# Kernel tuning notes

Hardware: AMD Instinct MI355X
Metric: run time of the kernel (lower is better)

The kernel has to match this reference:

```python
import jax, jax.numpy as jnp
import numpy as np

C = 512
NUM_HEADS = 8
NUM_GROUPS = 32
EPS = 1e-6


def group_norm(x, gamma, beta):
    # x: [B, C, N]
    b, c, n = x.shape
    xg = x.reshape(b, NUM_GROUPS, (c // NUM_GROUPS) * n)
    mean = xg.mean(axis=-1, keepdims=True)
    var = xg.var(axis=-1, keepdims=True)
    xg = (xg - mean) * jax.lax.rsqrt(var + EPS)
    x = xg.reshape(b, c, n)
    return x * gamma[None, :, None] + beta[None, :, None]


def conv1x1(x, w, bias):
    # pointwise conv: w [out_c, in_c], x [B, C, N]
    return jnp.einsum('oc,bcn->bon', w, x) + bias[None, :, None]


def setup_inputs() -> dict:
    key = jax.random.key(0)
    ks = jax.random.split(key, 11)
    s = 1.0 / np.sqrt(C)
    inp = {
        'x': jax.random.normal(ks[0], (4, C, 2048), dtype=jnp.float32),
        'gn_gamma': jnp.ones((C,), jnp.float32),
        'gn_beta': jnp.zeros((C,), jnp.float32),
        'q_w': jax.random.uniform(ks[1], (C, C), jnp.float32, -s, s),
        'q_b': jax.random.uniform(ks[2], (C,), jnp.float32, -s, s),
        'k_w': jax.random.uniform(ks[3], (C, C), jnp.float32, -s, s),
        'k_b': jax.random.uniform(ks[4], (C,), jnp.float32, -s, s),
        'v_w': jax.random.uniform(ks[5], (C, C), jnp.float32, -s, s),
        'v_b': jax.random.uniform(ks[6], (C,), jnp.float32, -s, s),
        'proj_w': jax.random.uniform(ks[7], (C, C), jnp.float32, -s, s),
        'proj_b': jax.random.uniform(ks[8], (C,), jnp.float32, -s, s),
    }
    return inp


def reference(x, gn_gamma, gn_beta, q_w, q_b, k_w, k_b, v_w, v_b, proj_w, proj_b):
    b, c, n = x.shape
    hc = c // NUM_HEADS
    h_ = group_norm(x, gn_gamma, gn_beta)
    q = conv1x1(h_, q_w, q_b)
    k = conv1x1(h_, k_w, k_b)
    v = conv1x1(h_, v_w, v_b)
    # split heads: [B, H, hc, N]
    q = q.reshape(b, NUM_HEADS, hc, n)
    k = k.reshape(b, NUM_HEADS, hc, n)
    v = v.reshape(b, NUM_HEADS, hc, n)
    # NOTE: scale uses full channel count c, matching the original code
    scale = jnp.asarray(c, x.dtype) ** -0.5
    # scores: [B, H, Nq, Nk]
    w = jnp.einsum('bhcn,bhcm->bhnm', q, k) * scale
    w = jax.nn.softmax(w, axis=-1)
    # out[b,h,c,q] = sum_m v[b,h,c,m] * w[b,h,q,m]
    out = jnp.einsum('bhcm,bhqm->bhcq', v, w)
    out = out.reshape(b, c, n)
    out = conv1x1(out, proj_w, proj_b)
    return x + out
```

## Files before the change

### kernel.cpp

```cpp
#include <hip/hip_runtime.h>
#include <hip/hip_bf16.h>
#include <math.h>

#define C_DIM 512
#define N_DIM 2048
#define B_DIM 4
#define NGRP 32
#define GCH 16
#define NHEAD 8
#define HDIM 64
#define EPSV 1e-6f

using f32x4  = __attribute__((ext_vector_type(4))) float;
using bf16x8 = __attribute__((ext_vector_type(8))) short;

#define GLL16(gp, lp) __builtin_amdgcn_global_load_lds( \
    (const __attribute__((address_space(1))) unsigned int*)(gp), \
    (__attribute__((address_space(3))) unsigned int*)(lp), 16, 0, 0)

#define BFPACK(a, b) __builtin_amdgcn_perm(__float_as_uint(b), __float_as_uint(a), 0x07060302u)

static __device__ __forceinline__ unsigned short f2bf(float f) {
    union { __hip_bfloat16 h; unsigned short u; } cv;
    cv.h = __float2bfloat16(f);
    return cv.u;
}

__global__ __launch_bounds__(256) void gn_stats(const float* __restrict__ x,
                                                float* __restrict__ partial) {
    const int HSZ = GCH * N_DIM / 2;
    int blk = blockIdx.x;
    const float4* x4 = (const float4*)(x + (size_t)blk * HSZ);
    int tid = threadIdx.x;

    float s = 0.f, ss = 0.f;
    #pragma unroll
    for (int it = 0; it < HSZ / 4 / 256; ++it) {
        float4 v = x4[tid + it * 256];
        s  += v.x + v.y + v.z + v.w;
        ss += v.x * v.x + v.y * v.y + v.z * v.z + v.w * v.w;
    }
    __shared__ float rs[256], rss[256];
    rs[tid] = s; rss[tid] = ss;
    __syncthreads();
    for (int off = 128; off > 0; off >>= 1) {
        if (tid < off) { rs[tid] += rs[tid + off]; rss[tid] += rss[tid + off]; }
        __syncthreads();
    }
    if (tid == 0) {
        partial[blk * 2]     = rs[0];
        partial[blk * 2 + 1] = rss[0];
    }
}

__global__ __launch_bounds__(256) void gn_apply_t(const float* __restrict__ x,
                                                  const float* __restrict__ partial,
                                                  const float* __restrict__ gamma,
                                                  const float* __restrict__ beta,
                                                  unsigned short* __restrict__ ht) {
    __shared__ char smem[8192];
    const float GSZI = 1.f / (GCH * N_DIM);
    int n0 = blockIdx.x * 64, c0 = blockIdx.y * 64, b = blockIdx.z;
    int tid = threadIdx.x;
    #pragma unroll
    for (int it = 0; it < 4; ++it) {
        int idx = tid + it * 256;
        int ci = idx >> 4, n4 = (idx & 15) << 2;
        int cg = c0 + ci, grp = cg >> 4;
        int bg = b * NGRP + grp;
        float s  = partial[bg * 4]     + partial[bg * 4 + 2];
        float ss = partial[bg * 4 + 1] + partial[bg * 4 + 3];
        float mean = s * GSZI;
        float var  = ss * GSZI - mean * mean;
        float rstd = rsqrtf(var + EPSV);
        float ga = gamma[cg] * rstd, be = beta[cg] - mean * ga;
        float4 v = *(const float4*)&x[((size_t)b * C_DIM + cg) * N_DIM + n0 + n4];
        float vals[4] = {v.x, v.y, v.z, v.w};
        #pragma unroll
        for (int j = 0; j < 4; ++j) {
            int nl = n4 + j;
            *(unsigned short*)(smem + nl * 128 + ((ci * 2) ^ ((nl & 7) << 4))) =
                f2bf(vals[j] * ga + be);
        }
    }
    __syncthreads();
    #pragma unroll
    for (int i = 0; i < 2; ++i) {
        int idx = tid + i * 256;
        int row = idx >> 3, ch = idx & 7;
        bf16x8 v = *(const bf16x8*)(smem + row * 128 + ((ch * 16) ^ ((row & 7) << 4)));
        *(bf16x8*)&ht[((size_t)(b * N_DIM + n0 + row)) * C_DIM + c0 + ch * 8] = v;
    }
}

__global__ __launch_bounds__(256) void cast4_bf16(const float* __restrict__ s0,
                                                  const float* __restrict__ s1,
                                                  const float* __restrict__ s2,
                                                  const float* __restrict__ s3,
                                                  unsigned short* __restrict__ dst) {
    int which = blockIdx.y;
    const float* src = (which == 0) ? s0 : (which == 1) ? s1 : (which == 2) ? s2 : s3;
    size_t idx = (size_t)blockIdx.x * 256 + threadIdx.x;
    const float4* s4 = (const float4*)src;
    float4 a = s4[idx * 2], b = s4[idx * 2 + 1];
    bf16x8 o;
    o[0] = (short)f2bf(a.x); o[1] = (short)f2bf(a.y);
    o[2] = (short)f2bf(a.z); o[3] = (short)f2bf(a.w);
    o[4] = (short)f2bf(b.x); o[5] = (short)f2bf(b.y);
    o[6] = (short)f2bf(b.z); o[7] = (short)f2bf(b.w);
    *(bf16x8*)&dst[(size_t)which * 262144 + idx * 8] = o;
}

__global__ __launch_bounds__(512) void conv_qkv(const unsigned short* __restrict__ Wall,
                                                const float* __restrict__ q_b,
                                                const float* __restrict__ k_b,
                                                const float* __restrict__ v_b,
                                                const unsigned short* __restrict__ ht,
                                                unsigned short* __restrict__ qt,
                                                unsigned short* __restrict__ kt,
                                                unsigned short* __restrict__ vt,
                                                float escale) {
    __shared__ char smem[40960];

    int bn0 = blockIdx.x * 128;
    int bo  = blockIdx.y * 64;
    int tid = threadIdx.x;
    int L = tid & 63, w = tid >> 6;
    int g = L >> 4, c = L & 15;
    int wr = w >> 2, wc = w & 3;

    f32x4 acc[3][2][2];
    #pragma unroll
    for (int w3 = 0; w3 < 3; ++w3)
        #pragma unroll
        for (int t = 0; t < 2; ++t)
            #pragma unroll
            for (int u = 0; u < 2; ++u) acc[w3][t][u] = f32x4{0.f, 0.f, 0.f, 0.f};

    for (int k0 = 0; k0 < C_DIM; k0 += 64) {
        if (w < 4) {
            #pragma unroll
            for (int i = 0; i < 4; ++i) {
                int j = w * 4 + i;
                int row = j * 8 + (L >> 3);
                int sl = (L & 7) ^ (row & 7);
                GLL16(ht + (size_t)(bn0 + row) * C_DIM + k0 + sl * 8, smem + j * 1024);
            }
        } else {
            #pragma unroll
            for (int i = 0; i < 6; ++i) {
                int j = (w - 4) * 6 + i;
                int w3 = j >> 3, jj = j & 7;
                int row = jj * 8 + (L >> 3);
                int sl = (L & 7) ^ (row & 7);
                GLL16(Wall + (size_t)w3 * 262144 + (size_t)(bo + row) * C_DIM + k0 + sl * 8,
                      smem + 16384 + j * 1024);
            }
        }
        __syncthreads();

        bf16x8 bfr[2][2];
        #pragma unroll
        for (int u = 0; u < 2; ++u) {
            int row = wc * 32 + u * 16 + c;
            #pragma unroll
            for (int ks = 0; ks < 2; ++ks)
                bfr[u][ks] = *(const bf16x8*)(smem + row * 128 +
                                              ((g * 16 + ks * 64) ^ ((row & 7) << 4)));
        }
        #pragma unroll
        for (int w3 = 0; w3 < 3; ++w3) {
            char* As = smem + 16384 + w3 * 8192;
            bf16x8 af[2][2];
            #pragma unroll
            for (int t = 0; t < 2; ++t) {
                int row = wr * 32 + t * 16 + c;
                #pragma unroll
                for (int ks = 0; ks < 2; ++ks)
                    af[t][ks] = *(const bf16x8*)(As + row * 128 +
                                                 ((g * 16 + ks * 64) ^ ((row & 7) << 4)));
            }
            #pragma unroll
            for (int ks = 0; ks < 2; ++ks)
                #pragma unroll
                for (int t = 0; t < 2; ++t)
                    #pragma unroll
                    for (int u = 0; u < 2; ++u)
                        acc[w3][t][u] = __builtin_amdgcn_mfma_f32_16x16x32_bf16(
                            af[t][ks], bfr[u][ks], acc[w3][t][u], 0, 0, 0);
        }
        __syncthreads();
    }

    int b  = bn0 >> 11;
    int nb = bn0 & (N_DIM - 1);
    int hh = bo >> 6;
    int bh = b * NHEAD + hh;

    #pragma unroll
    for (int t = 0; t < 2; ++t)
        #pragma unroll
        for (int r = 0; r < 4; ++r) {
            int m = bo + wr * 32 + t * 16 + g * 4 + r;
            float bi = v_b[m];
            #pragma unroll
            for (int u = 0; u < 2; ++u) {
                int n = nb + wc * 32 + u * 16 + c;
                vt[((size_t)b * C_DIM + m) * N_DIM + n] = f2bf(acc[2][t][u][r] + bi);
            }
        }

    char* Ts = smem;
    #pragma unroll
    for (int pass = 0; pass < 2; ++pass) {
        const float* bias = pass ? k_b : q_b;
        float esc = pass ? 1.0f : escale;
        unsigned short* dst = pass ? kt : qt;
        __syncthreads();
        #pragma unroll
        for (int t = 0; t < 2; ++t)
            #pragma unroll
            for (int r = 0; r < 4; ++r) {
                int ml = wr * 32 + t * 16 + g * 4 + r;
                float bi = bias[bo + ml];
                #pragma unroll
                for (int u = 0; u < 2; ++u) {
                    int nl = wc * 32 + u * 16 + c;
                    *(unsigned short*)(Ts + nl * 128 + ((ml * 2) ^ ((nl & 7) << 4))) =
                        f2bf((acc[pass][t][u][r] + bi) * esc);
                }
            }
        __syncthreads();
        #pragma unroll
        for (int i = 0; i < 2; ++i) {
            int idx = tid + i * 512;
            int row = idx >> 3, ch = idx & 7;
            bf16x8 v = *(const bf16x8*)(Ts + row * 128 + ((ch * 16) ^ ((row & 7) << 4)));
            *(bf16x8*)&dst[((size_t)bh * N_DIM + nb + row) * HDIM + ch * 8] = v;
        }
    }
}

__global__ __launch_bounds__(256) void conv_proj(const unsigned short* __restrict__ Wb,
                                                 const float* __restrict__ bias,
                                                 const unsigned short* __restrict__ Bsrc,
                                                 const float* __restrict__ res,
                                                 float* __restrict__ outf) {
    __shared__ char smem[24576];
    int bn0 = blockIdx.x * 128;
    int bo  = blockIdx.y * 64;
    int tid = threadIdx.x;
    int L = tid & 63, w = tid >> 6;
    int g = L >> 4, c = L & 15;
    int wr = w >> 1, wc = w & 1;

    f32x4 acc[2][4];
    #pragma unroll
    for (int t = 0; t < 2; ++t)
        #pragma unroll
        for (int u = 0; u < 4; ++u) acc[t][u] = f32x4{0.f, 0.f, 0.f, 0.f};

    for (int k0 = 0; k0 < C_DIM; k0 += 64) {
        #pragma unroll
        for (int i = 0; i < 2; ++i) {
            int j = w * 2 + i;
            int ra = j * 8 + (L >> 3);
            int sl = (L & 7) ^ (ra & 7);
            GLL16(Wb + (size_t)(bo + ra) * C_DIM + k0 + sl * 8, smem + j * 1024);
        }
        #pragma unroll
        for (int i = 0; i < 4; ++i) {
            int j = w * 4 + i;
            int rb = j * 8 + (L >> 3);
            int sl = (L & 7) ^ (rb & 7);
            GLL16(Bsrc + (size_t)(bn0 + rb) * C_DIM + k0 + sl * 8, smem + 8192 + j * 1024);
        }
        __syncthreads();

        bf16x8 af[2][2], bfr[4][2];
        #pragma unroll
        for (int t = 0; t < 2; ++t) {
            int row = wr * 32 + t * 16 + c;
            #pragma unroll
            for (int ks = 0; ks < 2; ++ks)
                af[t][ks] = *(const bf16x8*)(smem + row * 128 +
                                             ((g * 16 + ks * 64) ^ ((row & 7) << 4)));
        }
        #pragma unroll
        for (int u = 0; u < 4; ++u) {
            int row = wc * 64 + u * 16 + c;
            #pragma unroll
            for (int ks = 0; ks < 2; ++ks)
                bfr[u][ks] = *(const bf16x8*)(smem + 8192 + row * 128 +
                                              ((g * 16 + ks * 64) ^ ((row & 7) << 4)));
        }
        #pragma unroll
        for (int ks = 0; ks < 2; ++ks)
            #pragma unroll
            for (int t = 0; t < 2; ++t)
                #pragma unroll
                for (int u = 0; u < 4; ++u)
                    acc[t][u] = __builtin_amdgcn_mfma_f32_16x16x32_bf16(
                        af[t][ks], bfr[u][ks], acc[t][u], 0, 0, 0);
        __syncthreads();
    }

    int b  = bn0 >> 11;
    int nb = bn0 & (N_DIM - 1);
    #pragma unroll
    for (int t = 0; t < 2; ++t)
        #pragma unroll
        for (int r = 0; r < 4; ++r) {
            int m = bo + wr * 32 + t * 16 + g * 4 + r;
            float bi = bias[m];
            #pragma unroll
            for (int u = 0; u < 4; ++u) {
                int n = nb + wc * 64 + u * 16 + c;
                size_t off = ((size_t)b * C_DIM + m) * N_DIM + n;
                outf[off] = acc[t][u][r] + bi + res[off];
            }
        }
}

__global__ __launch_bounds__(256, 2) void attn_kernel(const unsigned short* __restrict__ Qt,
                                                      const unsigned short* __restrict__ Kt,
                                                      const unsigned short* __restrict__ Vt,
                                                      unsigned short* __restrict__ at) {
    __shared__ char smem[49152];

    int d = blockIdx.x;
    int xcd = d & 7;
    int slot = d >> 3;
    int bh = xcd + 8 * (slot >> 4);
    int q0 = (slot & 15) * 128;

    int b = bh >> 3, hh = bh & 7;
    int tid = threadIdx.x;
    int L = tid & 63, w = tid >> 6;
    int g = L >> 4, c = L & 15;

    const unsigned short* Qh = Qt + (size_t)bh * N_DIM * HDIM;
    const unsigned short* Kh = Kt + (size_t)bh * N_DIM * HDIM;
    const unsigned short* Vh = Vt + (size_t)bh * HDIM * N_DIM;

    int ssl = (L & 7) ^ (L >> 3);
    #pragma unroll
    for (int i = 0; i < 4; ++i) {
        int j = w * 4 + i;
        int row = j * 8 + (L >> 3);
        GLL16(Qh + (size_t)(q0 + row) * HDIM + ssl * 8, smem + j * 1024);
    }
    int srow = w * 16 + (L >> 3);
    GLL16(Kh + (size_t)srow * HDIM + ssl * 8,        smem + 16384 + (2 * w) * 1024);
    GLL16(Kh + (size_t)(srow + 8) * HDIM + ssl * 8,  smem + 16384 + (2 * w + 1) * 1024);
    GLL16(Vh + (size_t)srow * N_DIM + ssl * 8,       smem + 24576 + (2 * w) * 1024);
    GLL16(Vh + (size_t)(srow + 8) * N_DIM + ssl * 8, smem + 24576 + (2 * w + 1) * 1024);
    __syncthreads();

    int csw = (c & 7) << 4;
    char* kb0 = smem + 16384 + c * 128 + ((g * 16) ^ csw);
    char* kb1 = smem + 16384 + c * 128 + ((g * 16 + 64) ^ csw);
    char* pb  = smem + (w * 32 + c) * 128;
    int pwo0 = (g * 8) ^ csw;
    int pwo1 = (32 + g * 8) ^ csw;
    int pwo2 = (64 + g * 8) ^ csw;
    int pwo3 = (96 + g * 8) ^ csw;
    int pro0 = (g * 16) ^ csw;
    int pro1 = (64 + g * 16) ^ csw;

    bf16x8 qf[2][2];
    #pragma unroll
    for (int s = 0; s < 2; ++s) {
        qf[s][0] = *(const bf16x8*)(pb + s * 2048 + pro0);
        qf[s][1] = *(const bf16x8*)(pb + s * 2048 + pro1);
    }

    const unsigned short* kgp = Kh + (size_t)(64 + srow) * HDIM + ssl * 8;
    const unsigned short* vgp = Vh + (size_t)srow * N_DIM + 64 + ssl * 8;

    f32x4 oacc[2][4];
    #pragma unroll
    for (int s = 0; s < 2; ++s)
        #pragma unroll
        for (int t = 0; t < 4; ++t) oacc[s][t] = f32x4{0.f, 0.f, 0.f, 0.f};
    float m_r[2] = {-INFINITY, -INFINITY};
    float l_part[2] = {0.f, 0.f};

    auto tile = [&](int BOFF) {
        f32x4 sacc[2][4];
        #pragma unroll
        for (int s = 0; s < 2; ++s)
            #pragma unroll
            for (int t = 0; t < 4; ++t) sacc[s][t] = f32x4{0.f, 0.f, 0.f, 0.f};
        __builtin_amdgcn_s_setprio(1);
        #pragma unroll
        for (int t = 0; t < 4; ++t) {
            bf16x8 kf0 = *(const bf16x8*)(kb0 + BOFF + t * 2048);
            bf16x8 kf1 = *(const bf16x8*)(kb1 + BOFF + t * 2048);
            sacc[0][t] = __builtin_amdgcn_mfma_f32_16x16x32_bf16(kf0, qf[0][0], sacc[0][t], 0, 0, 0);
            sacc[0][t] = __builtin_amdgcn_mfma_f32_16x16x32_bf16(kf1, qf[0][1], sacc[0][t], 0, 0, 0);
            sacc[1][t] = __builtin_amdgcn_mfma_f32_16x16x32_bf16(kf0, qf[1][0], sacc[1][t], 0, 0, 0);
            sacc[1][t] = __builtin_amdgcn_mfma_f32_16x16x32_bf16(kf1, qf[1][1], sacc[1][t], 0, 0, 0);
        }
        __builtin_amdgcn_s_setprio(0);

        float mloc[2];
        #pragma unroll
        for (int s = 0; s < 2; ++s) {
            float t0 = fmaxf(fmaxf(sacc[s][0][0], sacc[s][0][1]), sacc[s][0][2]);
            float t1 = fmaxf(fmaxf(sacc[s][0][3], sacc[s][1][0]), sacc[s][1][1]);
            float t2 = fmaxf(fmaxf(sacc[s][1][2], sacc[s][1][3]), sacc[s][2][0]);
            float t3 = fmaxf(fmaxf(sacc[s][2][1], sacc[s][2][2]), sacc[s][2][3]);
            float t4 = fmaxf(fmaxf(sacc[s][3][0], sacc[s][3][1]), sacc[s][3][2]);
            mloc[s] = fmaxf(fmaxf(fmaxf(t0, t1), fmaxf(t2, t3)), fmaxf(t4, sacc[s][3][3]));
        }
        float growth = fmaxf(mloc[0] - m_r[0], mloc[1] - m_r[1]);
        if (!__all(growth <= 6.0f)) {
            #pragma unroll
            for (int s = 0; s < 2; ++s) {
                float ms = mloc[s];
                ms = fmaxf(ms, __shfl_xor(ms, 16));
                ms = fmaxf(ms, __shfl_xor(ms, 32));
                float mn = fmaxf(m_r[s], ms);
                float fac = exp2f(m_r[s] - mn);
                m_r[s] = mn;
                l_part[s] *= fac;
                #pragma unroll
                for (int t = 0; t < 4; ++t) oacc[s][t] = oacc[s][t] * fac;
            }
        }
        unsigned pk[2][4][2];
        #pragma unroll
        for (int s = 0; s < 2; ++s) {
            f32x4 m4 = {m_r[s], m_r[s], m_r[s], m_r[s]};
            f32x4 p[4];
            #pragma unroll
            for (int t = 0; t < 4; ++t) {
                f32x4 dd = sacc[s][t] - m4;
                p[t][0] = exp2f(dd[0]);
                p[t][1] = exp2f(dd[1]);
                p[t][2] = exp2f(dd[2]);
                p[t][3] = exp2f(dd[3]);
            }
            f32x4 racc = (p[0] + p[1]) + (p[2] + p[3]);
            l_part[s] += (racc[0] + racc[1]) + (racc[2] + racc[3]);
            #pragma unroll
            for (int t = 0; t < 4; ++t) {
                pk[s][t][0] = BFPACK(p[t][0], p[t][1]);
                pk[s][t][1] = BFPACK(p[t][2], p[t][3]);
            }
        }

        #pragma unroll
        for (int s = 0; s < 2; ++s) {
            char* sb = pb + s * 2048;
            *(unsigned long long*)(sb + pwo0) = (unsigned long long)pk[s][0][0] | ((unsigned long long)pk[s][0][1] << 32);
            *(unsigned long long*)(sb + pwo1) = (unsigned long long)pk[s][1][0] | ((unsigned long long)pk[s][1][1] << 32);
            *(unsigned long long*)(sb + pwo2) = (unsigned long long)pk[s][2][0] | ((unsigned long long)pk[s][2][1] << 32);
            *(unsigned long long*)(sb + pwo3) = (unsigned long long)pk[s][3][0] | ((unsigned long long)pk[s][3][1] << 32);
        }

        __builtin_amdgcn_s_setprio(1);
        #pragma unroll
        for (int ks = 0; ks < 2; ++ks) {
            char* kbase = (ks == 0 ? kb0 : kb1) + BOFF + 8192;
            bf16x8 pf0 = *(const bf16x8*)(pb + (ks ? pro1 : pro0));
            bf16x8 pf1 = *(const bf16x8*)(pb + 2048 + (ks ? pro1 : pro0));
            #pragma unroll
            for (int t = 0; t < 4; ++t) {
                bf16x8 vf = *(const bf16x8*)(kbase + t * 2048);
                oacc[0][t] = __builtin_amdgcn_mfma_f32_16x16x32_bf16(vf, pf0, oacc[0][t], 0, 0, 0);
                oacc[1][t] = __builtin_amdgcn_mfma_f32_16x16x32_bf16(vf, pf1, oacc[1][t], 0, 0, 0);
            }
        }
        __builtin_amdgcn_s_setprio(0);
    };

    #define ATTN_BARRIER() do { \
        __builtin_amdgcn_s_barrier(); \
        asm volatile("" ::: "memory"); \
    } while (0)
    #define ATTN_VMCNT4() do { \
        asm volatile("s_waitcnt vmcnt(4)" ::: "memory"); \
        __builtin_amdgcn_sched_barrier(0); \
    } while (0)
    #define ATTN_VMCNT0() do { \
        asm volatile("s_waitcnt vmcnt(0)" ::: "memory"); \
        __builtin_amdgcn_sched_barrier(0); \
    } while (0)

    for (int i = 0; i < 15; ++i) {
        ATTN_BARRIER();
        GLL16(kgp,              smem + 32768 + (2 * w) * 1024);
        GLL16(kgp + 8 * HDIM,   smem + 32768 + (2 * w + 1) * 1024);
        GLL16(vgp,              smem + 40960 + (2 * w) * 1024);
        GLL16(vgp + 8 * N_DIM,  smem + 40960 + (2 * w + 1) * 1024);
        kgp += 64 * HDIM;
        vgp += 64;
        ATTN_VMCNT4();
        tile(0);
        ATTN_BARRIER();
        GLL16(kgp,              smem + 16384 + (2 * w) * 1024);
        GLL16(kgp + 8 * HDIM,   smem + 16384 + (2 * w + 1) * 1024);
        GLL16(vgp,              smem + 24576 + (2 * w) * 1024);
        GLL16(vgp + 8 * N_DIM,  smem + 24576 + (2 * w + 1) * 1024);
        kgp += 64 * HDIM;
        vgp += 64;
        ATTN_VMCNT4();
        tile(16384);
    }
    ATTN_BARRIER();
    GLL16(kgp,              smem + 32768 + (2 * w) * 1024);
    GLL16(kgp + 8 * HDIM,   smem + 32768 + (2 * w + 1) * 1024);
    GLL16(vgp,              smem + 40960 + (2 * w) * 1024);
    GLL16(vgp + 8 * N_DIM,  smem + 40960 + (2 * w + 1) * 1024);
    ATTN_VMCNT4();
    tile(0);
    ATTN_BARRIER();
    ATTN_VMCNT0();
    tile(16384);

    #undef ATTN_BARRIER
    #undef ATTN_VMCNT4
    #undef ATTN_VMCNT0

    #pragma unroll
    for (int s = 0; s < 2; ++s) {
        float l_r = l_part[s];
        l_r += __shfl_xor(l_r, 16);
        l_r += __shfl_xor(l_r, 32);
        float oinv = 1.f / l_r;
        char* sb = pb + s * 2048;
        unsigned lo, hi;
        lo = BFPACK(oacc[s][0][0] * oinv, oacc[s][0][1] * oinv);
        hi = BFPACK(oacc[s][0][2] * oinv, oacc[s][0][3] * oinv);
        *(unsigned long long*)(sb + pwo0) = (unsigned long long)lo | ((unsigned long long)hi << 32);
        lo = BFPACK(oacc[s][1][0] * oinv, oacc[s][1][1] * oinv);
        hi = BFPACK(oacc[s][1][2] * oinv, oacc[s][1][3] * oinv);
        *(unsigned long long*)(sb + pwo1) = (unsigned long long)lo | ((unsigned long long)hi << 32);
        lo = BFPACK(oacc[s][2][0] * oinv, oacc[s][2][1] * oinv);
        hi = BFPACK(oacc[s][2][2] * oinv, oacc[s][2][3] * oinv);
        *(unsigned long long*)(sb + pwo2) = (unsigned long long)lo | ((unsigned long long)hi << 32);
        lo = BFPACK(oacc[s][3][0] * oinv, oacc[s][3][1] * oinv);
        hi = BFPACK(oacc[s][3][2] * oinv, oacc[s][3][3] * oinv);
        *(unsigned long long*)(sb + pwo3) = (unsigned long long)lo | ((unsigned long long)hi << 32);
    }
    char* wbase = smem + w * 4096;
    #pragma unroll
    for (int i = 0; i < 4; ++i) {
        int idx = L + i * 64;
        int row = idx >> 3, ch = idx & 7;
        bf16x8 v = *(const bf16x8*)(wbase + row * 128 + ((ch * 16) ^ ((row & 7) << 4)));
        *(bf16x8*)&at[((size_t)(b * N_DIM + q0 + w * 32 + row)) * C_DIM + hh * HDIM + ch * 8] = v;
    }
}

extern "C" void kernel_launch(void* const* d_in, const int* in_sizes, int n_in,
                              void* d_out, int out_size, void* d_ws, size_t ws_size,
                              hipStream_t stream) {
    (void)in_sizes; (void)n_in; (void)out_size; (void)ws_size;
    const float* x     = (const float*)d_in[0];
    const float* gam   = (const float*)d_in[1];
    const float* bet   = (const float*)d_in[2];
    const float* q_w   = (const float*)d_in[3];
    const float* q_b   = (const float*)d_in[4];
    const float* k_w   = (const float*)d_in[5];
    const float* k_b   = (const float*)d_in[6];
    const float* v_w   = (const float*)d_in[7];
    const float* v_b   = (const float*)d_in[8];
    const float* p_w   = (const float*)d_in[9];
    const float* p_b   = (const float*)d_in[10];
    float* out = (float*)d_out;

    const size_t MB = 1 << 20;
    char* wsb = (char*)d_ws;
    unsigned short* ht  = (unsigned short*)(wsb);
    unsigned short* wqb = (unsigned short*)(wsb + 8 * MB);
    unsigned short* wpb = (unsigned short*)(wsb + 9 * MB + 512 * 1024);
    float*          partial = (float*)(wsb + 10 * MB);
    unsigned short* qt  = (unsigned short*)(wsb + 11 * MB);
    unsigned short* kt  = (unsigned short*)(wsb + 19 * MB);
    unsigned short* vt  = (unsigned short*)(wsb + 27 * MB);
    unsigned short* at  = (unsigned short*)(wsb + 35 * MB);

    gn_stats<<<B_DIM * NGRP * 2, 256, 0, stream>>>(x, partial);
    gn_apply_t<<<dim3(N_DIM / 64, C_DIM / 64, B_DIM), 256, 0, stream>>>(x, partial, gam, bet, ht);

    cast4_bf16<<<dim3(128, 4), 256, 0, stream>>>(q_w, k_w, v_w, p_w, wqb);

    const float escale = 0.044194173824159216f * 1.4426950408889634f;
    conv_qkv<<<dim3(B_DIM * N_DIM / 128, C_DIM / 64), 512, 0, stream>>>(
        wqb, q_b, k_b, v_b, ht, qt, kt, vt, escale);

    attn_kernel<<<512, 256, 0, stream>>>(qt, kt, vt, at);

    conv_proj<<<dim3(B_DIM * N_DIM / 128, C_DIM / 64), 256, 0, stream>>>(wpb, p_b, at, x, out);
}
```

Before: 121.2 us.

## Switch attention to 32x32x16 MFMA and keep P in registers via permlane32 swap

Reworks the attention inner loop to use 32x32x16 bf16 MFMA tiles instead of 16x16x32 tiles, with each wave handling 32 query rows as one accumulator block. The softmax probabilities are now packed and rearranged across lane halves with v_permlane32_swap so they feed the PV MFMA directly from registers. This removes the LDS write/read round trip of P and halves the cross-lane reductions. In exchange it uses larger accumulator vectors (more VGPR pressure) and adds a block-wide sync before the output store.

```diff
diff --git a/kernel.cpp b/kernel.cpp
--- a/kernel.cpp
+++ b/kernel.cpp
@@ -12,6 +12,7 @@
 #define EPSV 1e-6f
 
 using f32x4  = __attribute__((ext_vector_type(4))) float;
+using f32x16 = __attribute__((ext_vector_type(16))) float;
 using bf16x8 = __attribute__((ext_vector_type(8))) short;
 
 #define GLL16(gp, lp) __builtin_amdgcn_global_load_lds( \
@@ -24,6 +25,19 @@
     union { __hip_bfloat16 h; unsigned short u; } cv;
     cv.h = __float2bfloat16(f);
     return cv.u;
+}
+
+static __device__ __forceinline__ f32x16 zero16() {
+    f32x16 z;
+    #pragma unroll
+    for (int i = 0; i < 16; ++i) z[i] = 0.f;
+    return z;
+}
+
+static __device__ __forceinline__ bf16x8 mk8(unsigned u0, unsigned u1, unsigned u2, unsigned u3) {
+    union { unsigned u[4]; bf16x8 v; } x;
+    x.u[0] = u0; x.u[1] = u1; x.u[2] = u2; x.u[3] = u3;
+    return x.v;
 }
 
 __global__ __launch_bounds__(256) void gn_stats(const float* __restrict__ x,
@@ -337,7 +351,7 @@
     int b = bh >> 3, hh = bh & 7;
     int tid = threadIdx.x;
     int L = tid & 63, w = tid >> 6;
-    int g = L >> 4, c = L & 15;
+    int c32 = L & 31, h = L >> 5;
 
     const unsigned short* Qh = Qt + (size_t)bh * N_DIM * HDIM;
     const unsigned short* Kh = Kt + (size_t)bh * N_DIM * HDIM;
@@ -357,121 +371,89 @@
     GLL16(Vh + (size_t)(srow + 8) * N_DIM + ssl * 8, smem + 24576 + (2 * w + 1) * 1024);
     __syncthreads();
 
-    int csw = (c & 7) << 4;
-    char* kb0 = smem + 16384 + c * 128 + ((g * 16) ^ csw);
-    char* kb1 = smem + 16384 + c * 128 + ((g * 16 + 64) ^ csw);
-    char* pb  = smem + (w * 32 + c) * 128;
-    int pwo0 = (g * 8) ^ csw;
-    int pwo1 = (32 + g * 8) ^ csw;
-    int pwo2 = (64 + g * 8) ^ csw;
-    int pwo3 = (96 + g * 8) ^ csw;
-    int pro0 = (g * 16) ^ csw;
-    int pro1 = (64 + g * 16) ^ csw;
-
-    bf16x8 qf[2][2];
-    #pragma unroll
-    for (int s = 0; s < 2; ++s) {
-        qf[s][0] = *(const bf16x8*)(pb + s * 2048 + pro0);
-        qf[s][1] = *(const bf16x8*)(pb + s * 2048 + pro1);
-    }
+    int kswz = (c32 & 7) << 4;
+    int ko[4];
+    #pragma unroll
+    for (int s = 0; s < 4; ++s) ko[s] = (h * 16 + 32 * s) ^ kswz;
+    char* rowK = smem + 16384 + c32 * 128;
+    char* strip = smem + (w * 32 + c32) * 128;
+
+    bf16x8 qf[4];
+    #pragma unroll
+    for (int s = 0; s < 4; ++s)
+        qf[s] = *(const bf16x8*)(strip + ko[s]);
 
     const unsigned short* kgp = Kh + (size_t)(64 + srow) * HDIM + ssl * 8;
     const unsigned short* vgp = Vh + (size_t)srow * N_DIM + 64 + ssl * 8;
 
-    f32x4 oacc[2][4];
-    #pragma unroll
-    for (int s = 0; s < 2; ++s)
-        #pragma unroll
-        for (int t = 0; t < 4; ++t) oacc[s][t] = f32x4{0.f, 0.f, 0.f, 0.f};
-    float m_r[2] = {-INFINITY, -INFINITY};
-    float l_part[2] = {0.f, 0.f};
+    f32x16 oacc0 = zero16(), oacc1 = zero16();
+    float m_r = -INFINITY, l_part = 0.f;
 
     auto tile = [&](int BOFF) {
-        f32x4 sacc[2][4];
-        #pragma unroll
-        for (int s = 0; s < 2; ++s)
-            #pragma unroll
-            for (int t = 0; t < 4; ++t) sacc[s][t] = f32x4{0.f, 0.f, 0.f, 0.f};
+        f32x16 sacc0 = zero16(), sacc1 = zero16();
         __builtin_amdgcn_s_setprio(1);
         #pragma unroll
-        for (int t = 0; t < 4; ++t) {
-            bf16x8 kf0 = *(const bf16x8*)(kb0 + BOFF + t * 2048);
-            bf16x8 kf1 = *(const bf16x8*)(kb1 + BOFF + t * 2048);
-            sacc[0][t] = __builtin_amdgcn_mfma_f32_16x16x32_bf16(kf0, qf[0][0], sacc[0][t], 0, 0, 0);
-            sacc[0][t] = __builtin_amdgcn_mfma_f32_16x16x32_bf16(kf1, qf[0][1], sacc[0][t], 0, 0, 0);
-            sacc[1][t] = __builtin_amdgcn_mfma_f32_16x16x32_bf16(kf0, qf[1][0], sacc[1][t], 0, 0, 0);
-            sacc[1][t] = __builtin_amdgcn_mfma_f32_16x16x32_bf16(kf1, qf[1][1], sacc[1][t], 0, 0, 0);
+        for (int s = 0; s < 4; ++s) {
+            bf16x8 kf0 = *(const bf16x8*)(rowK + BOFF + ko[s]);
+            bf16x8 kf1 = *(const bf16x8*)(rowK + BOFF + 4096 + ko[s]);
+            sacc0 = __builtin_amdgcn_mfma_f32_32x32x16_bf16(kf0, qf[s], sacc0, 0, 0, 0);
+            sacc1 = __builtin_amdgcn_mfma_f32_32x32x16_bf16(kf1, qf[s], sacc1, 0, 0, 0);
         }
         __builtin_amdgcn_s_setprio(0);
 
-        float mloc[2];
-        #pragma unroll
-        for (int s = 0; s < 2; ++s) {
-            float t0 = fmaxf(fmaxf(sacc[s][0][0], sacc[s][0][1]), sacc[s][0][2]);
-            float t1 = fmaxf(fmaxf(sacc[s][0][3], sacc[s][1][0]), sacc[s][1][1]);
-            float t2 = fmaxf(fmaxf(sacc[s][1][2], sacc[s][1][3]), sacc[s][2][0]);
-            float t3 = fmaxf(fmaxf(sacc[s][2][1], sacc[s][2][2]), sacc[s][2][3]);
-            float t4 = fmaxf(fmaxf(sacc[s][3][0], sacc[s][3][1]), sacc[s][3][2]);
-            mloc[s] = fmaxf(fmaxf(fmaxf(t0, t1), fmaxf(t2, t3)), fmaxf(t4, sacc[s][3][3]));
-        }
-        float growth = fmaxf(mloc[0] - m_r[0], mloc[1] - m_r[1]);
-        if (!__all(growth <= 6.0f)) {
-            #pragma unroll
-            for (int s = 0; s < 2; ++s) {
-                float ms = mloc[s];
-                ms = fmaxf(ms, __shfl_xor(ms, 16));
-                ms = fmaxf(ms, __shfl_xor(ms, 32));
-                float mn = fmaxf(m_r[s], ms);
-                float fac = exp2f(m_r[s] - mn);
-                m_r[s] = mn;
-                l_part[s] *= fac;
-                #pragma unroll
-                for (int t = 0; t < 4; ++t) oacc[s][t] = oacc[s][t] * fac;
-            }
-        }
-        unsigned pk[2][4][2];
-        #pragma unroll
-        for (int s = 0; s < 2; ++s) {
-            f32x4 m4 = {m_r[s], m_r[s], m_r[s], m_r[s]};
-            f32x4 p[4];
-            #pragma unroll
-            for (int t = 0; t < 4; ++t) {
-                f32x4 dd = sacc[s][t] - m4;
-                p[t][0] = exp2f(dd[0]);
-                p[t][1] = exp2f(dd[1]);
-                p[t][2] = exp2f(dd[2]);
-                p[t][3] = exp2f(dd[3]);
-            }
-            f32x4 racc = (p[0] + p[1]) + (p[2] + p[3]);
-            l_part[s] += (racc[0] + racc[1]) + (racc[2] + racc[3]);
-            #pragma unroll
-            for (int t = 0; t < 4; ++t) {
-                pk[s][t][0] = BFPACK(p[t][0], p[t][1]);
-                pk[s][t][1] = BFPACK(p[t][2], p[t][3]);
-            }
-        }
-
-        #pragma unroll
-        for (int s = 0; s < 2; ++s) {
-            char* sb = pb + s * 2048;
-            *(unsigned long long*)(sb + pwo0) = (unsigned long long)pk[s][0][0] | ((unsigned long long)pk[s][0][1] << 32);
-            *(unsigned long long*)(sb + pwo1) = (unsigned long long)pk[s][1][0] | ((unsigned long long)pk[s][1][1] << 32);
-            *(unsigned long long*)(sb + pwo2) = (unsigned long long)pk[s][2][0] | ((unsigned long long)pk[s][2][1] << 32);
-            *(unsigned long long*)(sb + pwo3) = (unsigned long long)pk[s][3][0] | ((unsigned long long)pk[s][3][1] << 32);
-        }
+        float mloc = -INFINITY;
+        #pragma unroll
+        for (int r = 0; r < 16; ++r) mloc = fmaxf(mloc, fmaxf(sacc0[r], sacc1[r]));
+        if (!__all(mloc - m_r <= 6.0f)) {
+            mloc = fmaxf(mloc, __shfl_xor(mloc, 32));
+            float mn = fmaxf(m_r, mloc);
+            float fac = exp2f(m_r - mn);
+            m_r = mn;
+            l_part *= fac;
+            oacc0 = oacc0 * fac;
+            oacc1 = oacc1 * fac;
+        }
+        bf16x8 pf[4];
+        float rs = 0.f;
+        {
+            float p[16];
+            #pragma unroll
+            for (int r = 0; r < 16; ++r) { p[r] = exp2f(sacc0[r] - m_r); rs += p[r]; }
+            unsigned a0 = BFPACK(p[0], p[1]),   bb0 = BFPACK(p[2], p[3]);
+            unsigned a1 = BFPACK(p[4], p[5]),   bb1 = BFPACK(p[6], p[7]);
+            unsigned a2 = BFPACK(p[8], p[9]),   bb2 = BFPACK(p[10], p[11]);
+            unsigned a3 = BFPACK(p[12], p[13]), bb3 = BFPACK(p[14], p[15]);
+            asm volatile("v_permlane32_swap_b32 %0, %1" : "+v"(a0), "+v"(a1));
+            asm volatile("v_permlane32_swap_b32 %0, %1" : "+v"(bb0), "+v"(bb1));
+            asm volatile("v_permlane32_swap_b32 %0, %1" : "+v"(a2), "+v"(a3));
+            asm volatile("v_permlane32_swap_b32 %0, %1" : "+v"(bb2), "+v"(bb3));
+            pf[0] = mk8(a0, bb0, a1, bb1);
+            pf[1] = mk8(a2, bb2, a3, bb3);
+        }
+        {
+            float p[16];
+            #pragma unroll
+            for (int r = 0; r < 16; ++r) { p[r] = exp2f(sacc1[r] - m_r); rs += p[r]; }
+            unsigned a0 = BFPACK(p[0], p[1]),   bb0 = BFPACK(p[2], p[3]);
+            unsigned a1 = BFPACK(p[4], p[5]),   bb1 = BFPACK(p[6], p[7]);
+            unsigned a2 = BFPACK(p[8], p[9]),   bb2 = BFPACK(p[10], p[11]);
+            unsigned a3 = BFPACK(p[12], p[13]), bb3 = BFPACK(p[14], p[15]);
+            asm volatile("v_permlane32_swap_b32 %0, %1" : "+v"(a0), "+v"(a1));
+            asm volatile("v_permlane32_swap_b32 %0, %1" : "+v"(bb0), "+v"(bb1));
+            asm volatile("v_permlane32_swap_b32 %0, %1" : "+v"(a2), "+v"(a3));
+            asm volatile("v_permlane32_swap_b32 %0, %1" : "+v"(bb2), "+v"(bb3));
+            pf[2] = mk8(a0, bb0, a1, bb1);
+            pf[3] = mk8(a2, bb2, a3, bb3);
+        }
+        l_part += rs;
 
         __builtin_amdgcn_s_setprio(1);
         #pragma unroll
-        for (int ks = 0; ks < 2; ++ks) {
-            char* kbase = (ks == 0 ? kb0 : kb1) + BOFF + 8192;
-            bf16x8 pf0 = *(const bf16x8*)(pb + (ks ? pro1 : pro0));
-            bf16x8 pf1 = *(const bf16x8*)(pb + 2048 + (ks ? pro1 : pro0));
-            #pragma unroll
-            for (int t = 0; t < 4; ++t) {
-                bf16x8 vf = *(const bf16x8*)(kbase + t * 2048);
-                oacc[0][t] = __builtin_amdgcn_mfma_f32_16x16x32_bf16(vf, pf0, oacc[0][t], 0, 0, 0);
-                oacc[1][t] = __builtin_amdgcn_mfma_f32_16x16x32_bf16(vf, pf1, oacc[1][t], 0, 0, 0);
-            }
+        for (int s = 0; s < 4; ++s) {
+            bf16x8 vf0 = *(const bf16x8*)(rowK + BOFF + 8192 + ko[s]);
+            bf16x8 vf1 = *(const bf16x8*)(rowK + BOFF + 8192 + 4096 + ko[s]);
+            oacc0 = __builtin_amdgcn_mfma_f32_32x32x16_bf16(vf0, pf[s], oacc0, 0, 0, 0);
+            oacc1 = __builtin_amdgcn_mfma_f32_32x32x16_bf16(vf1, pf[s], oacc1, 0, 0, 0);
         }
         __builtin_amdgcn_s_setprio(0);
     };
@@ -524,34 +506,26 @@
     #undef ATTN_VMCNT4
     #undef ATTN_VMCNT0
 
-    #pragma unroll
-    for (int s = 0; s < 2; ++s) {
-        float l_r = l_part[s];
-        l_r += __shfl_xor(l_r, 16);
-        l_r += __shfl_xor(l_r, 32);
-        float oinv = 1.f / l_r;
-        char* sb = pb + s * 2048;
-        unsigned lo, hi;
-        lo = BFPACK(oacc[s][0][0] * oinv, oacc[s][0][1] * oinv);
-        hi = BFPACK(oacc[s][0][2] * oinv, oacc[s][0][3] * oinv);
-        *(unsigned long long*)(sb + pwo0) = (unsigned long long)lo | ((unsigned long long)hi << 32);
-        lo = BFPACK(oacc[s][1][0] * oinv, oacc[s][1][1] * oinv);
-        hi = BFPACK(oacc[s][1][2] * oinv, oacc[s][1][3] * oinv);
-        *(unsigned long long*)(sb + pwo1) = (unsigned long long)lo | ((unsigned long long)hi << 32);
-        lo = BFPACK(oacc[s][2][0] * oinv, oacc[s][2][1] * oinv);
-        hi = BFPACK(oacc[s][2][2] * oinv, oacc[s][2][3] * oinv);
-        *(unsigned long long*)(sb + pwo2) = (unsigned long long)lo | ((unsigned long long)hi << 32);
-        lo = BFPACK(oacc[s][3][0] * oinv, oacc[s][3][1] * oinv);
-        hi = BFPACK(oacc[s][3][2] * oinv, oacc[s][3][3] * oinv);
-        *(unsigned long long*)(sb + pwo3) = (unsigned long long)lo | ((unsigned long long)hi << 32);
-    }
-    char* wbase = smem + w * 4096;
+    float l_r = l_part + __shfl_xor(l_part, 32);
+    float oinv = 1.f / l_r;
+    #pragma unroll
+    for (int db = 0; db < 2; ++db) {
+        const f32x16& o = db ? oacc1 : oacc0;
+        #pragma unroll
+        for (int j = 0; j < 4; ++j) {
+            unsigned lo = BFPACK(o[4 * j] * oinv,     o[4 * j + 1] * oinv);
+            unsigned hi = BFPACK(o[4 * j + 2] * oinv, o[4 * j + 3] * oinv);
+            *(unsigned long long*)(strip + ((db * 64 + h * 8 + 16 * j) ^ kswz)) =
+                (unsigned long long)lo | ((unsigned long long)hi << 32);
+        }
+    }
+    __syncthreads();
     #pragma unroll
     for (int i = 0; i < 4; ++i) {
-        int idx = L + i * 64;
+        int idx = tid + i * 256;
         int row = idx >> 3, ch = idx & 7;
-        bf16x8 v = *(const bf16x8*)(wbase + row * 128 + ((ch * 16) ^ ((row & 7) << 4)));
-        *(bf16x8*)&at[((size_t)(b * N_DIM + q0 + w * 32 + row)) * C_DIM + hh * HDIM + ch * 8] = v;
+        bf16x8 v = *(const bf16x8*)(smem + row * 128 + ((ch * 16) ^ ((row & 7) << 4)));
+        *(bf16x8*)&at[((size_t)(b * N_DIM + q0 + row)) * C_DIM + hh * HDIM + ch * 8] = v;
     }
 }
 
```

Result: faster. 116.4 us (-4.0%).
